# Optimization experiments

Hardware: AMD Instinct MI355X
Metric: run time of the kernel (lower is better)

The kernel has to match this reference:

```python
import jax, jax.numpy as jnp
import numpy as np

N, E, IN, H, C, OUT = 50000, 800000, 128, 4, 32, 40
HID = H * C  # 128


def _layernorm(x, g, b, eps=1e-5):
    mu = x.mean(-1, keepdims=True)
    var = ((x - mu) ** 2).mean(-1, keepdims=True)
    return (x - mu) * jax.lax.rsqrt(var + eps) * g + b


def _gatv2(x, src, dst, Wl, bl, Wr, br, att, bias, heads, ch, concat):
    n = x.shape[0]
    xl = (x @ Wl + bl).reshape(n, heads, ch)  # source-side transform
    xr = (x @ Wr + br).reshape(n, heads, ch)  # target-side transform
    e = jax.nn.leaky_relu(xl[src] + xr[dst], 0.2)          # [E,H,C]
    alpha = jnp.einsum('ehc,hc->eh', e, att)                # [E,H]
    m = jax.ops.segment_max(alpha, dst, num_segments=n)
    m = jnp.where(jnp.isfinite(m), m, 0.0)
    a = jnp.exp(alpha - m[dst])
    denom = jax.ops.segment_sum(a, dst, num_segments=n)
    a = a / (denom[dst] + 1e-16)
    out = jax.ops.segment_sum(xl[src] * a[:, :, None], dst, num_segments=n)  # [N,H,C]
    out = out.reshape(n, heads * ch) if concat else out.mean(1)
    return out + bias


def setup_inputs():
    key = jax.random.key(0)
    ks = jax.random.split(key, 26)
    s = 0.05
    rn = lambda k, sh: jax.random.normal(k, sh, jnp.float32) * s
    inp = {
        'x': jax.random.normal(ks[0], (N, IN), jnp.float32),
        'edge_index': jax.random.randint(ks[1], (2, E), 0, N, jnp.int64),
        'W0': rn(ks[2], (IN, HID)), 'b0': jnp.zeros((HID,), jnp.float32),
        'W1l': rn(ks[3], (IN, HID)), 'b1l': jnp.zeros((HID,), jnp.float32),
        'W1r': rn(ks[4], (IN, HID)), 'b1r': jnp.zeros((HID,), jnp.float32),
        'att1': rn(ks[5], (H, C)), 'bias1': jnp.zeros((HID,), jnp.float32),
        'g1': jnp.ones((HID,), jnp.float32), 'be1': jnp.zeros((HID,), jnp.float32),
        'W2l': rn(ks[6], (HID, HID)), 'b2l': jnp.zeros((HID,), jnp.float32),
        'W2r': rn(ks[7], (HID, HID)), 'b2r': jnp.zeros((HID,), jnp.float32),
        'att2': rn(ks[8], (H, C)), 'bias2': jnp.zeros((HID,), jnp.float32),
        'g2': jnp.ones((HID,), jnp.float32), 'be2': jnp.zeros((HID,), jnp.float32),
        'W3l': rn(ks[9], (HID, OUT)), 'b3l': jnp.zeros((OUT,), jnp.float32),
        'W3r': rn(ks[10], (HID, OUT)), 'b3r': jnp.zeros((OUT,), jnp.float32),
        'att3': rn(ks[11], (1, OUT)), 'bias3': jnp.zeros((OUT,), jnp.float32),
    }
    return inp


def reference(x, edge_index, W0, b0, W1l, b1l, W1r, b1r, att1, bias1, g1, be1,
              W2l, b2l, W2r, b2r, att2, bias2, g2, be2,
              W3l, b3l, W3r, b3r, att3, bias3):
    src, dst = edge_index[0], edge_index[1]
    identity = x @ W0 + b0
    out = _gatv2(x, src, dst, W1l, b1l, W1r, b1r, att1, bias1, H, C, True)
    out = jax.nn.gelu(_layernorm(out, g1, be1), approximate=False)
    x1 = out + identity  # dropout is identity in eval mode
    out = _gatv2(x1, src, dst, W2l, b2l, W2r, b2r, att2, bias2, H, C, True)
    out = jax.nn.gelu(_layernorm(out, g2, be2), approximate=False)
    x2 = out + x1
    return _gatv2(x2, src, dst, W3l, b3l, W3r, b3r, att3, bias3, 1, OUT, False)
```

## Files before the change

### kernel.cpp

```cpp
#include <hip/hip_runtime.h>
#include <hip/hip_bf16.h>

#define NN 50000
#define EE 800000
#define OUTD 40
#define NBUCK 196
#define BCAP 8192
#define ABLKS 400
#define EPB 2000

typedef __attribute__((ext_vector_type(8))) short short8;
typedef __attribute__((ext_vector_type(4))) float floatx4;

__device__ __forceinline__ float bf2f(unsigned short u) {
  union { unsigned int i; float f; } v; v.i = ((unsigned int)u) << 16; return v.f;
}
__device__ __forceinline__ unsigned short f2bf(float f) {
  union { float f; unsigned int i; } v; v.f = f;
  unsigned int x = v.i;
  return (unsigned short)((x + 0x7fffu + ((x >> 16) & 1u)) >> 16);
}
__device__ __forceinline__ float blo(unsigned int u) {
  union { unsigned int i; float f; } v; v.i = u << 16; return v.f;
}
__device__ __forceinline__ float bhi(unsigned int u) {
  union { unsigned int i; float f; } v; v.i = u & 0xffff0000u; return v.f;
}

template <int CTRL>
__device__ __forceinline__ float dpp_add(float x) {
  int y = __builtin_amdgcn_update_dpp(0, __float_as_int(x), CTRL, 0xF, 0xF, true);
  return x + __int_as_float(y);
}

__device__ __forceinline__ float gelu1(float y) {
  float y2 = y * y;
  float z = y * fmaf(0.0356774081f, y2, 0.7978845608f);
  float e = __expf(-2.f * z);
  float r = __builtin_amdgcn_rcpf(1.f + e);
  float th = fmaf(2.f, r, -1.f);
  return y * fmaf(0.5f, th, 0.5f);
}

__device__ __forceinline__ int clampe(int i, int last) {
  int r = i <= last ? i : last;
  return r < 0 ? 0 : r;
}

__device__ __forceinline__ int probe_f32(const void* x) {
  int lane = threadIdx.x & 63;
  unsigned short u = ((const unsigned short*)x)[2 * lane];
  int exf = (u >> 7) & 0xFF;
  unsigned long long b = __ballot((exf >= 100 && exf <= 142) ? 1 : 0);
  return (__popcll(b) >= 48) ? 0 : 1;
}
__device__ __forceinline__ int probe_i64(const void* ei) {
  int lane = threadIdx.x & 63;
  long long v = ((const long long*)ei)[lane];
  unsigned long long b = __ballot((v >= 0 && v < NN) ? 1 : 0);
  return (__popcll(b) >= 48) ? 1 : 0;
}

struct WDesc { const void* W; unsigned short* F; int T; int ncols; };
struct WDescs { WDesc d[7]; int cum[8]; };
struct PCv { const void* s; unsigned short* d; int n; int cap; };
struct PCvs { PCv a[17]; };

__global__ __launch_bounds__(256) void init_kernel(const void* __restrict__ ei,
                                                   const void* __restrict__ x,
                                                   int* __restrict__ flags,
                                                   int* __restrict__ bcur,
                                                   WDescs ds, PCvs P) {
  int b = blockIdx.x;
  int f32 = probe_f32(x);
  if (b < 48) {
    int idx = b * 256 + threadIdx.x;
    if (idx >= 12288) return;
    int mi = 0;
    while (idx >= ds.cum[mi + 1]) mi++;
    int local = idx - ds.cum[mi];
    WDesc d = ds.d[mi];
    int lane = local & 63;
    int rest = local >> 6;
    int t = rest % d.T;
    int kb = rest / d.T;
    int m = lane & 15, quad = lane >> 4;
    int col = t * 16 + m;
    short8 v;
    for (int j = 0; j < 8; ++j) {
      int k = kb * 32 + quad * 8 + j;
      if (col < d.ncols) {
        int off = k * d.ncols + col;
        v[j] = f32 ? (short)f2bf(((const float*)d.W)[off])
                   : (short)((const unsigned short*)d.W)[off];
      } else {
        v[j] = 0;
      }
    }
    *(short8*)(d.F + (size_t)local * 8) = v;
  } else if (b < 65) {
    PCv p = P.a[b - 48];
    for (int i = threadIdx.x; i < p.cap; i += 256) {
      unsigned short o = 0;
      if (i < p.n)
        o = f32 ? f2bf(((const float*)p.s)[i]) : ((const unsigned short*)p.s)[i];
      p.d[i] = o;
    }
  } else {
    for (int i = threadIdx.x; i < NBUCK * 16; i += 256) bcur[i] = 0;
    if (threadIdx.x < 64) {
      int i64 = probe_i64(ei);
      if (threadIdx.x == 0) {
        flags[0] = i64;
        flags[1] = f32;
        flags[2] = 0;
      }
    }
  }
}

struct GSet { const unsigned short* F; const unsigned short* bias; unsigned short* Out; };
struct GArgs { GSet s[3]; };

__device__ __forceinline__ short8 pack_f4(float4 u0, float4 u1) {
  short8 r;
  r[0] = (short)f2bf(u0.x); r[1] = (short)f2bf(u0.y);
  r[2] = (short)f2bf(u0.z); r[3] = (short)f2bf(u0.w);
  r[4] = (short)f2bf(u1.x); r[5] = (short)f2bf(u1.y);
  r[6] = (short)f2bf(u1.z); r[7] = (short)f2bf(u1.w);
  return r;
}

__device__ __forceinline__ void gemm_body(int wave, int lane, const void* __restrict__ A,
                                          int f32, const GArgs& g, int nset, int M,
                                          int T, int ncols) {
  int r0 = wave * 16;
  if (r0 >= M) return;
  int m = lane & 15, quad = lane >> 4;
  short8 a0, a1, a2, a3;
  if (!f32) {
    const unsigned short* ar = (const unsigned short*)A + (size_t)(r0 + m) * 128 + quad * 8;
    a0 = *(const short8*)(ar);
    a1 = *(const short8*)(ar + 32);
    a2 = *(const short8*)(ar + 64);
    a3 = *(const short8*)(ar + 96);
  } else {
    const float* ar = (const float*)A + (size_t)(r0 + m) * 128 + quad * 8;
    a0 = pack_f4(*(const float4*)(ar), *(const float4*)(ar + 4));
    a1 = pack_f4(*(const float4*)(ar + 32), *(const float4*)(ar + 36));
    a2 = pack_f4(*(const float4*)(ar + 64), *(const float4*)(ar + 68));
    a3 = pack_f4(*(const float4*)(ar + 96), *(const float4*)(ar + 100));
  }
  size_t kstride = (size_t)T * 64 * 8;
  for (int si = 0; si < nset; ++si) {
    const unsigned short* F = g.s[si].F;
    const unsigned short* bias = g.s[si].bias;
    unsigned short* Out = g.s[si].Out;
    for (int t = 0; t < T; ++t) {
      floatx4 acc = {0.f, 0.f, 0.f, 0.f};
      const unsigned short* wp = F + ((size_t)t * 64 + lane) * 8;
      acc = __builtin_amdgcn_mfma_f32_16x16x32_bf16(a0, *(const short8*)(wp), acc, 0, 0, 0);
      acc = __builtin_amdgcn_mfma_f32_16x16x32_bf16(a1, *(const short8*)(wp + kstride), acc, 0, 0, 0);
      acc = __builtin_amdgcn_mfma_f32_16x16x32_bf16(a2, *(const short8*)(wp + 2 * kstride), acc, 0, 0, 0);
      acc = __builtin_amdgcn_mfma_f32_16x16x32_bf16(a3, *(const short8*)(wp + 3 * kstride), acc, 0, 0, 0);
      int col = t * 16 + m;
      if (col < ncols) {
        float bb = bf2f(bias[col]);
        for (int r = 0; r < 4; ++r) {
          int row = r0 + quad * 4 + r;
          Out[(size_t)row * ncols + col] = f2bf(acc[r] + bb);
        }
      }
    }
  }
}

__global__ __launch_bounds__(256) void gemm_multi_kernel(
    const void* __restrict__ A, const int* __restrict__ flagp, GArgs g,
    int nset, int M, int T, int ncols) {
  int wave = blockIdx.x * 4 + (threadIdx.x >> 6);
  int lane = threadIdx.x & 63;
  gemm_body(wave, lane, A, *flagp, g, nset, M, T, ncols);
}

__global__ __launch_bounds__(512) void fused_scatter_gemm(
    const void* __restrict__ ei, unsigned int* __restrict__ bedges,
    int* __restrict__ bcur, const void* __restrict__ A,
    const int* __restrict__ flagp, GArgs g, int nset, int M, int T, int ncols) {
  __shared__ int lhist[NBUCK];
  __shared__ int lbase[NBUCK];
  if (blockIdx.x >= ABLKS) {
    int wave = (blockIdx.x - ABLKS) * 8 + (threadIdx.x >> 6);
    gemm_body(wave, threadIdx.x & 63, A, *flagp, g, nset, M, T, ncols);
    return;
  }
  int tid = threadIdx.x;
  if (tid < NBUCK) lhist[tid] = 0;
  int i64 = probe_i64(ei);
  __syncthreads();
  int e0 = blockIdx.x * EPB;
  int e1 = e0 + EPB; if (e1 > EE) e1 = EE;
  for (int e = e0 + tid; e < e1; e += 512) {
    int d = i64 ? (int)((const long long*)ei)[EE + e] : ((const int*)ei)[EE + e];
    d = d < 0 ? 0 : (d >= NN ? NN - 1 : d);
    atomicAdd(&lhist[d >> 8], 1);
  }
  __syncthreads();
  if (tid < NBUCK) {
    int c = lhist[tid];
    lbase[tid] = c ? atomicAdd(&bcur[tid * 16], c) : 0;
    lhist[tid] = 0;
  }
  __syncthreads();
  for (int e = e0 + tid; e < e1; e += 512) {
    int s, d;
    if (i64) {
      s = (int)((const long long*)ei)[e];
      d = (int)((const long long*)ei)[EE + e];
    } else {
      s = ((const int*)ei)[e];
      d = ((const int*)ei)[EE + e];
    }
    s = s < 0 ? 0 : (s >= NN ? NN - 1 : s);
    d = d < 0 ? 0 : (d >= NN ? NN - 1 : d);
    int bin = d >> 8;
    int r = atomicAdd(&lhist[bin], 1);
    int pos = lbase[bin] + r;
    if (pos < BCAP)
      bedges[(size_t)bin * BCAP + pos] =
          ((unsigned int)(d & 0xFF) << 24) | ((unsigned int)s << 8);
  }
}

__global__ __launch_bounds__(512) void fused_sort_gemm(
    const unsigned int* __restrict__ bedges, const int* __restrict__ bcur,
    int* __restrict__ offs, int* __restrict__ src_sorted,
    const void* __restrict__ A, const int* __restrict__ flagp, GArgs g,
    int nset, int M, int T, int ncols) {
  __shared__ int lhist[256];
  __shared__ int lscan[256];
  __shared__ int lbin[256];
  __shared__ int sbase, scount, stotal;
  __shared__ unsigned int le[BCAP];
  __shared__ unsigned short lrank[BCAP];
  if (blockIdx.x >= NBUCK) {
    int wave = (blockIdx.x - NBUCK) * 8 + (threadIdx.x >> 6);
    gemm_body(wave, threadIdx.x & 63, A, *flagp, g, nset, M, T, ncols);
    return;
  }
  int k = blockIdx.x;
  int tid = threadIdx.x;
  if (tid < 256) {
    int c = 0;
    if (tid < NBUCK) {
      int v = bcur[tid * 16];
      c = v < BCAP ? v : BCAP;
    }
    lscan[tid] = c;
  }
  __syncthreads();
  for (int off = 1; off < 256; off <<= 1) {
    int u = 0;
    if (tid < 256 && tid >= off) u = lscan[tid - off];
    __syncthreads();
    if (tid < 256) lscan[tid] += u;
    __syncthreads();
  }
  if (tid == 0) {
    int pb = (k == 0) ? 0 : lscan[k - 1];
    sbase = pb;
    scount = lscan[k] - pb;
    stotal = lscan[NBUCK - 1];
  }
  if (tid < 256) lhist[tid] = 0;
  __syncthreads();
  int base = sbase, count = scount;
  const unsigned int* myb = bedges + (size_t)k * BCAP;
  for (int i = tid; i < count; i += 512) {
    unsigned int pk = myb[i];
    int bin = pk >> 24;
    int r = atomicAdd(&lhist[bin], 1);
    le[i] = pk;
    lrank[i] = (unsigned short)r;
  }
  __syncthreads();
  int hc = 0;
  if (tid < 256) {
    hc = lhist[tid];
    lscan[tid] = hc;
  }
  __syncthreads();
  for (int off = 1; off < 256; off <<= 1) {
    int u = 0;
    if (tid < 256 && tid >= off) u = lscan[tid - off];
    __syncthreads();
    if (tid < 256) lscan[tid] += u;
    __syncthreads();
  }
  if (tid < 256) {
    int binoff = lscan[tid] - hc;
    lbin[tid] = binoff;
    int node = k * 256 + tid;
    if (node < NN) offs[node] = base + binoff;
    if (k == 0 && tid == 0) offs[NN] = stotal;
  }
  __syncthreads();
  for (int i = tid; i < count; i += 512) {
    unsigned int pk = le[i];
    int bin = pk >> 24;
    int pos = base + lbin[bin] + (int)lrank[i];
    src_sorted[pos] = (int)(pk & 0x00FFFF00u);
  }
}

__global__ __launch_bounds__(256) void edge_hid_kernel(
    const unsigned short* __restrict__ xl, const unsigned short* __restrict__ xr,
    const unsigned short* __restrict__ att, const unsigned short* __restrict__ bias,
    const unsigned short* __restrict__ gamma, const unsigned short* __restrict__ beta,
    const unsigned short* __restrict__ resid, unsigned short* __restrict__ xout,
    const int* __restrict__ offs, const int* __restrict__ srcs) {
  int wpair = blockIdx.x * 4 + (threadIdx.x >> 6);
  int lane = threadIdx.x & 63;
  int half = lane >> 5;
  int wv = wpair * 2 + half;
  if (wv >= NN) return;
  int hl = lane & 31;
  int sub = hl >> 4;
  int cb = (hl & 15) * 16;
  int beg = offs[wv], end = offs[wv + 1], last = end - 1;
  int iters = (end - beg + 1) >> 1;
  int oi = __shfl_xor(iters, 32);
  int maxit = __builtin_amdgcn_readfirstlane(iters > oi ? iters : oi);
  const char* xlb = (const char*)xl;
  int c0 = hl * 4;
  uint2 rr = *(const uint2*)(resid + (size_t)wv * 128 + c0);
  uint4 xr8 = *(const uint4*)((const char*)xr + (size_t)wv * 256 + cb);
  float rx0 = blo(xr8.x), rx1 = bhi(xr8.x), rx2 = blo(xr8.y), rx3 = bhi(xr8.y);
  float rx4 = blo(xr8.z), rx5 = bhi(xr8.z), rx6 = blo(xr8.w), rx7 = bhi(xr8.w);
  uint4 at8 = *(const uint4*)((const char*)att + cb);
  float a0 = blo(at8.x), a1 = bhi(at8.x), a2 = blo(at8.y), a3 = bhi(at8.y);
  float a4 = blo(at8.z), a5 = bhi(at8.z), a6 = blo(at8.w), a7 = bhi(at8.w);
  float acc0 = 0.f, acc1 = 0.f, acc2 = 0.f, acc3 = 0.f;
  float acc4 = 0.f, acc5 = 0.f, acc6 = 0.f, acc7 = 0.f, den = 0.f;
  int ir = beg + sub;
  int o_cur = srcs[clampe(ir, last)];
  int o_nxt = srcs[clampe(ir + 2, last)];
  uint4 u = *(const uint4*)(xlb + (o_cur + cb));
  for (int it = 0; it < maxit; ++it) {
    int o_p = srcs[clampe(ir + 4, last)];
    uint4 un = *(const uint4*)(xlb + (o_nxt + cb));
    float mk = (ir <= last) ? 1.f : 0.f;
    ir += 2;
    float x0 = blo(u.x), x1 = bhi(u.x), x2 = blo(u.y), x3 = bhi(u.y);
    float x4 = blo(u.z), x5 = bhi(u.z), x6 = blo(u.w), x7 = bhi(u.w);
    float t0 = x0 + rx0, t1 = x1 + rx1, t2 = x2 + rx2, t3 = x3 + rx3;
    float t4 = x4 + rx4, t5 = x5 + rx5, t6 = x6 + rx6, t7 = x7 + rx7;
    float pa = a0 * t0;
    pa = fmaf(a1, t1, pa); pa = fmaf(a2, t2, pa); pa = fmaf(a3, t3, pa);
    pa = fmaf(a4, t4, pa); pa = fmaf(a5, t5, pa); pa = fmaf(a6, t6, pa); pa = fmaf(a7, t7, pa);
    float pb = a0 * fabsf(t0);
    pb = fmaf(a1, fabsf(t1), pb); pb = fmaf(a2, fabsf(t2), pb); pb = fmaf(a3, fabsf(t3), pb);
    pb = fmaf(a4, fabsf(t4), pb); pb = fmaf(a5, fabsf(t5), pb);
    pb = fmaf(a6, fabsf(t6), pb); pb = fmaf(a7, fabsf(t7), pb);
    float p = fmaf(0.4f, pb, 0.6f * pa);
    p = dpp_add<0xB1>(p);
    p = dpp_add<0x4E>(p);
    float w = __expf(fminf(p, 60.f)) * mk;
    den += w;
    acc0 = fmaf(w, x0, acc0); acc1 = fmaf(w, x1, acc1);
    acc2 = fmaf(w, x2, acc2); acc3 = fmaf(w, x3, acc3);
    acc4 = fmaf(w, x4, acc4); acc5 = fmaf(w, x5, acc5);
    acc6 = fmaf(w, x6, acc6); acc7 = fmaf(w, x7, acc7);
    u = un;
    o_nxt = o_p;
  }
  den += __shfl_xor(den, 16);
  acc0 += __shfl_xor(acc0, 16); acc1 += __shfl_xor(acc1, 16);
  acc2 += __shfl_xor(acc2, 16); acc3 += __shfl_xor(acc3, 16);
  acc4 += __shfl_xor(acc4, 16); acc5 += __shfl_xor(acc5, 16);
  acc6 += __shfl_xor(acc6, 16); acc7 += __shfl_xor(acc7, 16);
  int srcLane = (half << 5) + (hl >> 1);
  float b0 = __shfl(acc0, srcLane), b1 = __shfl(acc1, srcLane);
  float b2 = __shfl(acc2, srcLane), b3 = __shfl(acc3, srcLane);
  float h4 = __shfl(acc4, srcLane), h5 = __shfl(acc5, srcLane);
  float h6 = __shfl(acc6, srcLane), h7 = __shfl(acc7, srcLane);
  float dn = __shfl(den, srcLane);
  bool hi = (hl & 1) != 0;
  float v0 = hi ? h4 : b0, v1 = hi ? h5 : b1, v2 = hi ? h6 : b2, v3 = hi ? h7 : b3;
  float inv = __builtin_amdgcn_rcpf(dn + 1e-16f);
  uint2 bb = *(const uint2*)(bias + c0);
  float o0 = v0 * inv + blo(bb.x), o1 = v1 * inv + bhi(bb.x);
  float o2 = v2 * inv + blo(bb.y), o3 = v3 * inv + bhi(bb.y);
  float s = (o0 + o1) + (o2 + o3);
  for (int k = 1; k < 32; k <<= 1) s += __shfl_xor(s, k);
  float mu = s * (1.f / 128.f);
  float d0 = o0 - mu, d1 = o1 - mu, d2 = o2 - mu, d3 = o3 - mu;
  float q = (d0 * d0 + d1 * d1) + (d2 * d2 + d3 * d3);
  for (int k = 1; k < 32; k <<= 1) q += __shfl_xor(q, k);
  float rstd = rsqrtf(q * (1.f / 128.f) + 1e-5f);
  uint2 gg = *(const uint2*)(gamma + c0);
  uint2 be = *(const uint2*)(beta + c0);
  float y0 = d0 * rstd * blo(gg.x) + blo(be.x);
  float y1 = d1 * rstd * bhi(gg.x) + bhi(be.x);
  float y2 = d2 * rstd * blo(gg.y) + blo(be.y);
  float y3 = d3 * rstd * bhi(gg.y) + bhi(be.y);
  y0 = gelu1(y0); y1 = gelu1(y1); y2 = gelu1(y2); y3 = gelu1(y3);
  y0 += blo(rr.x); y1 += bhi(rr.x); y2 += blo(rr.y); y3 += bhi(rr.y);
  uint2 pk;
  pk.x = (unsigned int)f2bf(y0) | ((unsigned int)f2bf(y1) << 16);
  pk.y = (unsigned int)f2bf(y2) | ((unsigned int)f2bf(y3) << 16);
  *(uint2*)(xout + (size_t)wv * 128 + c0) = pk;
}

__global__ __launch_bounds__(256) void edge_out_kernel(
    const unsigned short* __restrict__ xl, const unsigned short* __restrict__ xr,
    const unsigned short* __restrict__ att, const unsigned short* __restrict__ bias,
    void* __restrict__ out, const int* __restrict__ flagp,
    const int* __restrict__ offs, const int* __restrict__ srcs) {
  int wv = blockIdx.x * 4 + (threadIdx.x >> 6);
  if (wv >= NN) return;
  int lane = threadIdx.x & 63;
  int oct = lane >> 3;
  int cb = (lane & 7) * 16;
  int beg = __builtin_amdgcn_readfirstlane(offs[wv]);
  int last = __builtin_amdgcn_readfirstlane(offs[wv + 1]) - 1;
  const char* xlb = (const char*)xl;
  uint4 xr8 = *(const uint4*)((const char*)xr + (size_t)wv * 128 + cb);
  float rx0 = blo(xr8.x), rx1 = bhi(xr8.x), rx2 = blo(xr8.y), rx3 = bhi(xr8.y);
  float rx4 = blo(xr8.z), rx5 = bhi(xr8.z), rx6 = blo(xr8.w), rx7 = bhi(xr8.w);
  uint4 at8 = *(const uint4*)((const char*)att + cb);
  float a0 = blo(at8.x), a1 = bhi(at8.x), a2 = blo(at8.y), a3 = bhi(at8.y);
  float a4 = blo(at8.z), a5 = bhi(at8.z), a6 = blo(at8.w), a7 = bhi(at8.w);
  float acc0 = 0.f, acc1 = 0.f, acc2 = 0.f, acc3 = 0.f;
  float acc4 = 0.f, acc5 = 0.f, acc6 = 0.f, acc7 = 0.f, den = 0.f;
  int ir = beg + oct;
  int o_cur = srcs[clampe(ir, last)];
  int o_nxt = srcs[clampe(ir + 8, last)];
  uint4 u = *(const uint4*)(xlb + ((o_cur >> 1) + cb));
  for (int e = beg; e <= last; e += 8) {
    int o_p = srcs[clampe(ir + 16, last)];
    uint4 un = *(const uint4*)(xlb + ((o_nxt >> 1) + cb));
    float mk = (ir <= last) ? 1.f : 0.f;
    ir += 8;
    float x0 = blo(u.x), x1 = bhi(u.x), x2 = blo(u.y), x3 = bhi(u.y);
    float x4 = blo(u.z), x5 = bhi(u.z), x6 = blo(u.w), x7 = bhi(u.w);
    float t0 = x0 + rx0, t1 = x1 + rx1, t2 = x2 + rx2, t3 = x3 + rx3;
    float t4 = x4 + rx4, t5 = x5 + rx5, t6 = x6 + rx6, t7 = x7 + rx7;
    float pa = a0 * t0;
    pa = fmaf(a1, t1, pa); pa = fmaf(a2, t2, pa); pa = fmaf(a3, t3, pa);
    pa = fmaf(a4, t4, pa); pa = fmaf(a5, t5, pa); pa = fmaf(a6, t6, pa); pa = fmaf(a7, t7, pa);
    float pb = a0 * fabsf(t0);
    pb = fmaf(a1, fabsf(t1), pb); pb = fmaf(a2, fabsf(t2), pb); pb = fmaf(a3, fabsf(t3), pb);
    pb = fmaf(a4, fabsf(t4), pb); pb = fmaf(a5, fabsf(t5), pb);
    pb = fmaf(a6, fabsf(t6), pb); pb = fmaf(a7, fabsf(t7), pb);
    float p = fmaf(0.4f, pb, 0.6f * pa);
    p = dpp_add<0xB1>(p);
    p = dpp_add<0x4E>(p);
    p = dpp_add<0x141>(p);
    float w = __expf(fminf(p, 60.f)) * mk;
    den += w;
    acc0 = fmaf(w, x0, acc0); acc1 = fmaf(w, x1, acc1);
    acc2 = fmaf(w, x2, acc2); acc3 = fmaf(w, x3, acc3);
    acc4 = fmaf(w, x4, acc4); acc5 = fmaf(w, x5, acc5);
    acc6 = fmaf(w, x6, acc6); acc7 = fmaf(w, x7, acc7);
    u = un;
    o_nxt = o_p;
  }
  den += __shfl_xor(den, 8);  den += __shfl_xor(den, 16);  den += __shfl_xor(den, 32);
  acc0 += __shfl_xor(acc0, 8); acc0 += __shfl_xor(acc0, 16); acc0 += __shfl_xor(acc0, 32);
  acc1 += __shfl_xor(acc1, 8); acc1 += __shfl_xor(acc1, 16); acc1 += __shfl_xor(acc1, 32);
  acc2 += __shfl_xor(acc2, 8); acc2 += __shfl_xor(acc2, 16); acc2 += __shfl_xor(acc2, 32);
  acc3 += __shfl_xor(acc3, 8); acc3 += __shfl_xor(acc3, 16); acc3 += __shfl_xor(acc3, 32);
  acc4 += __shfl_xor(acc4, 8); acc4 += __shfl_xor(acc4, 16); acc4 += __shfl_xor(acc4, 32);
  acc5 += __shfl_xor(acc5, 8); acc5 += __shfl_xor(acc5, 16); acc5 += __shfl_xor(acc5, 32);
  acc6 += __shfl_xor(acc6, 8); acc6 += __shfl_xor(acc6, 16); acc6 += __shfl_xor(acc6, 32);
  acc7 += __shfl_xor(acc7, 8); acc7 += __shfl_xor(acc7, 16); acc7 += __shfl_xor(acc7, 32);
  float inv = __builtin_amdgcn_rcpf(den + 1e-16f);
  if (lane < 5) {
    uint4 bb = *(const uint4*)((const char*)bias + cb);
    float v0 = acc0 * inv + blo(bb.x), v1 = acc1 * inv + bhi(bb.x);
    float v2 = acc2 * inv + blo(bb.y), v3 = acc3 * inv + bhi(bb.y);
    float v4 = acc4 * inv + blo(bb.z), v5 = acc5 * inv + bhi(bb.z);
    float v6 = acc6 * inv + blo(bb.w), v7 = acc7 * inv + bhi(bb.w);
    int c0 = lane * 8;
    if (*flagp) {
      float* op = (float*)out + (size_t)wv * OUTD + c0;
      float4 f0 = {v0, v1, v2, v3};
      float4 f1 = {v4, v5, v6, v7};
      *(float4*)(op) = f0;
      *(float4*)(op + 4) = f1;
    } else {
      uint4 pk;
      pk.x = (unsigned int)f2bf(v0) | ((unsigned int)f2bf(v1) << 16);
      pk.y = (unsigned int)f2bf(v2) | ((unsigned int)f2bf(v3) << 16);
      pk.z = (unsigned int)f2bf(v4) | ((unsigned int)f2bf(v5) << 16);
      pk.w = (unsigned int)f2bf(v6) | ((unsigned int)f2bf(v7) << 16);
      *(uint4*)((unsigned short*)out + (size_t)wv * OUTD + c0) = pk;
    }
  }
}

extern "C" void kernel_launch(void* const* d_in, const int* in_sizes, int n_in,
                              void* d_out, int out_size, void* d_ws, size_t ws_size,
                              hipStream_t stream) {
  const void* x = d_in[0];
  const void* ei = d_in[1];

  char* ws = (char*)d_ws;
  size_t o = 0;
  auto alloc = [&](size_t bytes) {
    void* p = ws + o;
    o = (o + bytes + 255) & ~(size_t)255;
    return p;
  };
  int* flags = (int*)alloc(256);
  int* src_sorted = (int*)alloc((size_t)EE * 4);
  int* offs = (int*)alloc((size_t)(NN + 1) * 4);
  int* bcur = (int*)alloc((size_t)NBUCK * 16 * 4);
  unsigned int* bedges = (unsigned int*)alloc((size_t)NBUCK * BCAP * 4);
  unsigned short* F_W0 = (unsigned short*)alloc(2048 * 16);
  unsigned short* F_W1l = (unsigned short*)alloc(2048 * 16);
  unsigned short* F_W1r = (unsigned short*)alloc(2048 * 16);
  unsigned short* F_W2l = (unsigned short*)alloc(2048 * 16);
  unsigned short* F_W2r = (unsigned short*)alloc(2048 * 16);
  unsigned short* F_W3l = (unsigned short*)alloc(1024 * 16);
  unsigned short* F_W3r = (unsigned short*)alloc(1024 * 16);
  unsigned short* pblk = (unsigned short*)alloc(4096);
  unsigned short* ident = (unsigned short*)alloc((size_t)NN * 128 * 2);
  unsigned short* bxl = (unsigned short*)alloc((size_t)NN * 128 * 2);
  unsigned short* bxr = (unsigned short*)alloc((size_t)NN * 128 * 2);
  (void)ws_size;

  unsigned short* pb0 = pblk;
  unsigned short* pb1l = pblk + 128;
  unsigned short* pb1r = pblk + 256;
  unsigned short* patt1 = pblk + 384;
  unsigned short* pbias1 = pblk + 512;
  unsigned short* pg1 = pblk + 640;
  unsigned short* pbe1 = pblk + 768;
  unsigned short* pb2l = pblk + 896;
  unsigned short* pb2r = pblk + 1024;
  unsigned short* patt2 = pblk + 1152;
  unsigned short* pbias2 = pblk + 1280;
  unsigned short* pg2 = pblk + 1408;
  unsigned short* pbe2 = pblk + 1536;
  unsigned short* pb3l = pblk + 1664;
  unsigned short* pb3r = pblk + 1728;
  unsigned short* patt3 = pblk + 1792;
  unsigned short* pbias3 = pblk + 1856;

  WDescs wd;
  wd.d[0] = {d_in[2], F_W0, 8, 128};
  wd.d[1] = {d_in[4], F_W1l, 8, 128};
  wd.d[2] = {d_in[6], F_W1r, 8, 128};
  wd.d[3] = {d_in[12], F_W2l, 8, 128};
  wd.d[4] = {d_in[14], F_W2r, 8, 128};
  wd.d[5] = {d_in[20], F_W3l, 4, 40};
  wd.d[6] = {d_in[22], F_W3r, 4, 40};
  int cum[8] = {0, 2048, 4096, 6144, 8192, 10240, 11264, 12288};
  for (int i = 0; i < 8; ++i) wd.cum[i] = cum[i];
  PCvs P;
  P.a[0] = {d_in[3], pb0, 128, 128};
  P.a[1] = {d_in[5], pb1l, 128, 128};
  P.a[2] = {d_in[7], pb1r, 128, 128};
  P.a[3] = {d_in[8], patt1, 128, 128};
  P.a[4] = {d_in[9], pbias1, 128, 128};
  P.a[5] = {d_in[10], pg1, 128, 128};
  P.a[6] = {d_in[11], pbe1, 128, 128};
  P.a[7] = {d_in[13], pb2l, 128, 128};
  P.a[8] = {d_in[15], pb2r, 128, 128};
  P.a[9] = {d_in[16], patt2, 128, 128};
  P.a[10] = {d_in[17], pbias2, 128, 128};
  P.a[11] = {d_in[18], pg2, 128, 128};
  P.a[12] = {d_in[19], pbe2, 128, 128};
  P.a[13] = {d_in[21], pb3l, 40, 64};
  P.a[14] = {d_in[23], pb3r, 40, 64};
  P.a[15] = {d_in[24], patt3, 40, 64};
  P.a[16] = {d_in[25], pbias3, 40, 64};
  init_kernel<<<66, 256, 0, stream>>>(ei, x, flags, bcur, wd, P);

  const int* fx = flags + 1;
  const int* f0 = flags + 2;
  const int gb8 = (NN + 127) / 128;
  const int gb4 = (NN / 16 + 3) / 4;
  const int eb = (NN + 3) / 4;
  const int eb2 = (NN / 2 + 3) / 4;

  GArgs gi; gi.s[0] = {F_W0, pb0, ident};
  gi.s[1] = {nullptr, nullptr, nullptr}; gi.s[2] = {nullptr, nullptr, nullptr};
  fused_scatter_gemm<<<ABLKS + gb8, 512, 0, stream>>>(ei, bedges, bcur, x, fx, gi, 1,
                                                      NN, 8, 128);

  GArgs g1a; g1a.s[0] = {F_W1l, pb1l, bxl}; g1a.s[1] = {F_W1r, pb1r, bxr};
  g1a.s[2] = {nullptr, nullptr, nullptr};
  fused_sort_gemm<<<NBUCK + gb8, 512, 0, stream>>>(bedges, bcur, offs, src_sorted, x,
                                                   fx, g1a, 2, NN, 8, 128);

  edge_hid_kernel<<<eb2, 256, 0, stream>>>(bxl, bxr, patt1, pbias1, pg1, pbe1, ident,
                                           ident, offs, src_sorted);

  GArgs g2a; g2a.s[0] = {F_W2l, pb2l, bxl}; g2a.s[1] = {F_W2r, pb2r, bxr};
  g2a.s[2] = {nullptr, nullptr, nullptr};
  gemm_multi_kernel<<<gb4, 256, 0, stream>>>(ident, f0, g2a, 2, NN, 8, 128);
  edge_hid_kernel<<<eb2, 256, 0, stream>>>(bxl, bxr, patt2, pbias2, pg2, pbe2, ident,
                                           ident, offs, src_sorted);

  GArgs g3a; g3a.s[0] = {F_W3l, pb3l, bxl}; g3a.s[1] = {F_W3r, pb3r, bxr};
  g3a.s[2] = {nullptr, nullptr, nullptr};
  gemm_multi_kernel<<<gb4, 256, 0, stream>>>(ident, f0, g3a, 2, NN, 4, 64);
  edge_out_kernel<<<eb, 256, 0, stream>>>(bxl, bxr, patt3, pbias3, d_out, fx, offs,
                                          src_sorted);
}
```

Before: 306.4 us.

## Cache bf16 copy of x and vectorize GEMM output stores via swapped MFMA operands

The first GEMM, which reads the fp32 input x, now also writes a bf16 copy of x to a new workspace buffer. The second fused GEMM reads that copy, so it moves half the bytes and skips re-packing. The MFMA operands are swapped so each lane holds four consecutive output columns of one row. The epilogue can then load the bias as one uint2 and write four packed bf16 values per lane in a single 8-byte store, replacing four strided 2-byte stores. The cost is an extra 12.8MB write in the first kernel and a dependency on kernel ordering for the cache.

Result: slower. 322.3 us (+5.2%).

```diff
diff --git a/kernel.cpp b/kernel.cpp
--- a/kernel.cpp
+++ b/kernel.cpp
@@ -133,7 +133,8 @@
 
 __device__ __forceinline__ void gemm_body(int wave, int lane, const void* __restrict__ A,
                                           int f32, const GArgs& g, int nset, int M,
-                                          int T, int ncols) {
+                                          int T, int ncols,
+                                          unsigned short* __restrict__ Acache) {
   int r0 = wave * 16;
   if (r0 >= M) return;
   int m = lane & 15, quad = lane >> 4;
@@ -150,6 +151,13 @@
     a1 = pack_f4(*(const float4*)(ar + 32), *(const float4*)(ar + 36));
     a2 = pack_f4(*(const float4*)(ar + 64), *(const float4*)(ar + 68));
     a3 = pack_f4(*(const float4*)(ar + 96), *(const float4*)(ar + 100));
+    if (Acache) {
+      unsigned short* cp = Acache + (size_t)(r0 + m) * 128 + quad * 8;
+      *(short8*)(cp) = a0;
+      *(short8*)(cp + 32) = a1;
+      *(short8*)(cp + 64) = a2;
+      *(short8*)(cp + 96) = a3;
+    }
   }
   size_t kstride = (size_t)T * 64 * 8;
   for (int si = 0; si < nset; ++si) {
@@ -159,17 +167,19 @@
     for (int t = 0; t < T; ++t) {
       floatx4 acc = {0.f, 0.f, 0.f, 0.f};
       const unsigned short* wp = F + ((size_t)t * 64 + lane) * 8;
-      acc = __builtin_amdgcn_mfma_f32_16x16x32_bf16(a0, *(const short8*)(wp), acc, 0, 0, 0);
-      acc = __builtin_amdgcn_mfma_f32_16x16x32_bf16(a1, *(const short8*)(wp + kstride), acc, 0, 0, 0);
-      acc = __builtin_amdgcn_mfma_f32_16x16x32_bf16(a2, *(const short8*)(wp + 2 * kstride), acc, 0, 0, 0);
-      acc = __builtin_amdgcn_mfma_f32_16x16x32_bf16(a3, *(const short8*)(wp + 3 * kstride), acc, 0, 0, 0);
-      int col = t * 16 + m;
-      if (col < ncols) {
-        float bb = bf2f(bias[col]);
-        for (int r = 0; r < 4; ++r) {
-          int row = r0 + quad * 4 + r;
-          Out[(size_t)row * ncols + col] = f2bf(acc[r] + bb);
-        }
+      acc = __builtin_amdgcn_mfma_f32_16x16x32_bf16(*(const short8*)(wp), a0, acc, 0, 0, 0);
+      acc = __builtin_amdgcn_mfma_f32_16x16x32_bf16(*(const short8*)(wp + kstride), a1, acc, 0, 0, 0);
+      acc = __builtin_amdgcn_mfma_f32_16x16x32_bf16(*(const short8*)(wp + 2 * kstride), a2, acc, 0, 0, 0);
+      acc = __builtin_amdgcn_mfma_f32_16x16x32_bf16(*(const short8*)(wp + 3 * kstride), a3, acc, 0, 0, 0);
+      int cbase = t * 16 + quad * 4;
+      if (cbase < ncols) {
+        uint2 bb = *(const uint2*)(bias + cbase);
+        float v0 = acc[0] + blo(bb.x), v1 = acc[1] + bhi(bb.x);
+        float v2 = acc[2] + blo(bb.y), v3 = acc[3] + bhi(bb.y);
+        uint2 pk;
+        pk.x = (unsigned int)f2bf(v0) | ((unsigned int)f2bf(v1) << 16);
+        pk.y = (unsigned int)f2bf(v2) | ((unsigned int)f2bf(v3) << 16);
+        *(uint2*)(Out + (size_t)(r0 + m) * ncols + cbase) = pk;
       }
     }
   }
@@ -180,18 +190,21 @@
     int nset, int M, int T, int ncols) {
   int wave = blockIdx.x * 4 + (threadIdx.x >> 6);
   int lane = threadIdx.x & 63;
-  gemm_body(wave, lane, A, *flagp, g, nset, M, T, ncols);
+  gemm_body(wave, lane, A, *flagp, g, nset, M, T, ncols, nullptr);
 }
 
 __global__ __launch_bounds__(512) void fused_scatter_gemm(
     const void* __restrict__ ei, unsigned int* __restrict__ bedges,
     int* __restrict__ bcur, const void* __restrict__ A,
-    const int* __restrict__ flagp, GArgs g, int nset, int M, int T, int ncols) {
+    const int* __restrict__ flagp, GArgs g, int nset, int M, int T, int ncols,
+    unsigned short* __restrict__ Acache) {
   __shared__ int lhist[NBUCK];
   __shared__ int lbase[NBUCK];
   if (blockIdx.x >= ABLKS) {
     int wave = (blockIdx.x - ABLKS) * 8 + (threadIdx.x >> 6);
-    gemm_body(wave, threadIdx.x & 63, A, *flagp, g, nset, M, T, ncols);
+    int f32 = *flagp;
+    gemm_body(wave, threadIdx.x & 63, A, f32, g, nset, M, T, ncols,
+              f32 ? Acache : nullptr);
     return;
   }
   int tid = threadIdx.x;
@@ -236,7 +249,7 @@
     const unsigned int* __restrict__ bedges, const int* __restrict__ bcur,
     int* __restrict__ offs, int* __restrict__ src_sorted,
     const void* __restrict__ A, const int* __restrict__ flagp, GArgs g,
-    int nset, int M, int T, int ncols) {
+    int nset, int M, int T, int ncols, const unsigned short* __restrict__ Acache) {
   __shared__ int lhist[256];
   __shared__ int lscan[256];
   __shared__ int lbin[256];
@@ -245,7 +258,9 @@
   __shared__ unsigned short lrank[BCAP];
   if (blockIdx.x >= NBUCK) {
     int wave = (blockIdx.x - NBUCK) * 8 + (threadIdx.x >> 6);
-    gemm_body(wave, threadIdx.x & 63, A, *flagp, g, nset, M, T, ncols);
+    int f32 = *flagp;
+    const void* Ause = f32 ? (const void*)Acache : A;
+    gemm_body(wave, threadIdx.x & 63, Ause, 0, g, nset, M, T, ncols, nullptr);
     return;
   }
   int k = blockIdx.x;
@@ -529,6 +544,7 @@
   unsigned short* ident = (unsigned short*)alloc((size_t)NN * 128 * 2);
   unsigned short* bxl = (unsigned short*)alloc((size_t)NN * 128 * 2);
   unsigned short* bxr = (unsigned short*)alloc((size_t)NN * 128 * 2);
+  unsigned short* xbf = (unsigned short*)alloc((size_t)NN * 128 * 2);
   (void)ws_size;
 
   unsigned short* pb0 = pblk;
@@ -589,12 +605,12 @@
   GArgs gi; gi.s[0] = {F_W0, pb0, ident};
   gi.s[1] = {nullptr, nullptr, nullptr}; gi.s[2] = {nullptr, nullptr, nullptr};
   fused_scatter_gemm<<<ABLKS + gb8, 512, 0, stream>>>(ei, bedges, bcur, x, fx, gi, 1,
-                                                      NN, 8, 128);
+                                                      NN, 8, 128, xbf);
 
   GArgs g1a; g1a.s[0] = {F_W1l, pb1l, bxl}; g1a.s[1] = {F_W1r, pb1r, bxr};
   g1a.s[2] = {nullptr, nullptr, nullptr};
   fused_sort_gemm<<<NBUCK + gb8, 512, 0, stream>>>(bedges, bcur, offs, src_sorted, x,
-                                                   fx, g1a, 2, NN, 8, 128);
+                                                   fx, g1a, 2, NN, 8, 128, xbf);
 
   edge_hid_kernel<<<eb2, 256, 0, stream>>>(bxl, bxr, patt1, pbias1, pg1, pbe1, ident,
                                            ident, offs, src_sorted);
```

## Fuse next-layer GEMMs into edge_hid epilogue with ping-pong buffers

Applied to the files above, without the earlier changes.

Each edge_hid block now stages its 8 normalized output rows in shared memory, zero-padded to 16 rows. It then runs MFMA against the next layer's left and right weight fragments, writing the next xl/xr directly. This removes the two standalone gemm_multi launches and the global round-trip of the activation matrix, and skips writing x2 since nothing downstream reads it. In exchange, every block re-reads the full weight fragments from cache and wastes half of each 16-row MFMA tile. Ping-pong xl/xr buffers avoid overwriting inputs still being gathered by other blocks.

Result: no change. 306.6 us (+0.1%).

```diff
diff --git a/kernel.cpp b/kernel.cpp
--- a/kernel.cpp
+++ b/kernel.cpp
@@ -175,14 +175,6 @@
   }
 }
 
-__global__ __launch_bounds__(256) void gemm_multi_kernel(
-    const void* __restrict__ A, const int* __restrict__ flagp, GArgs g,
-    int nset, int M, int T, int ncols) {
-  int wave = blockIdx.x * 4 + (threadIdx.x >> 6);
-  int lane = threadIdx.x & 63;
-  gemm_body(wave, lane, A, *flagp, g, nset, M, T, ncols);
-}
-
 __global__ __launch_bounds__(512) void fused_scatter_gemm(
     const void* __restrict__ ei, unsigned int* __restrict__ bedges,
     int* __restrict__ bcur, const void* __restrict__ A,
@@ -313,17 +305,21 @@
   }
 }
 
+template <int TT, int NCOLS, int WRITEX>
 __global__ __launch_bounds__(256) void edge_hid_kernel(
     const unsigned short* __restrict__ xl, const unsigned short* __restrict__ xr,
     const unsigned short* __restrict__ att, const unsigned short* __restrict__ bias,
     const unsigned short* __restrict__ gamma, const unsigned short* __restrict__ beta,
     const unsigned short* __restrict__ resid, unsigned short* __restrict__ xout,
-    const int* __restrict__ offs, const int* __restrict__ srcs) {
+    const int* __restrict__ offs, const int* __restrict__ srcs,
+    const unsigned short* __restrict__ Fl, const unsigned short* __restrict__ Fr,
+    const unsigned short* __restrict__ bl, const unsigned short* __restrict__ br,
+    unsigned short* __restrict__ outl, unsigned short* __restrict__ outr) {
+  __shared__ unsigned short sA[16 * 128];
   int wpair = blockIdx.x * 4 + (threadIdx.x >> 6);
   int lane = threadIdx.x & 63;
   int half = lane >> 5;
   int wv = wpair * 2 + half;
-  if (wv >= NN) return;
   int hl = lane & 31;
   int sub = hl >> 4;
   int cb = (hl & 15) * 16;
@@ -409,7 +405,44 @@
   uint2 pk;
   pk.x = (unsigned int)f2bf(y0) | ((unsigned int)f2bf(y1) << 16);
   pk.y = (unsigned int)f2bf(y2) | ((unsigned int)f2bf(y3) << 16);
-  *(uint2*)(xout + (size_t)wv * 128 + c0) = pk;
+  if (WRITEX) *(uint2*)(xout + (size_t)wv * 128 + c0) = pk;
+
+  int lrow = (threadIdx.x >> 6) * 2 + half;
+  *(uint2*)(&sA[lrow * 128 + c0]) = pk;
+  *(uint2*)(&sA[1024 + threadIdx.x * 4]) = make_uint2(0, 0);
+  __syncthreads();
+  int m = lane & 15, quad = lane >> 4;
+  const unsigned short* arow = sA + m * 128 + quad * 8;
+  short8 A0 = *(const short8*)(arow);
+  short8 A1 = *(const short8*)(arow + 32);
+  short8 A2 = *(const short8*)(arow + 64);
+  short8 A3 = *(const short8*)(arow + 96);
+  const size_t kst = (size_t)TT * 64 * 8;
+  const int rowbase = blockIdx.x * 8;
+  const int wid = threadIdx.x >> 6;
+  constexpr int PER = (2 * TT) / 4;
+#pragma unroll
+  for (int jj = 0; jj < PER; ++jj) {
+    int j = wid * PER + jj;
+    bool isr = j >= TT;
+    const unsigned short* F = isr ? Fr : Fl;
+    const unsigned short* bs = isr ? br : bl;
+    unsigned short* Out = isr ? outr : outl;
+    int t = isr ? j - TT : j;
+    floatx4 acc = {0.f, 0.f, 0.f, 0.f};
+    const unsigned short* wp = F + ((size_t)t * 64 + lane) * 8;
+    acc = __builtin_amdgcn_mfma_f32_16x16x32_bf16(A0, *(const short8*)(wp), acc, 0, 0, 0);
+    acc = __builtin_amdgcn_mfma_f32_16x16x32_bf16(A1, *(const short8*)(wp + kst), acc, 0, 0, 0);
+    acc = __builtin_amdgcn_mfma_f32_16x16x32_bf16(A2, *(const short8*)(wp + 2 * kst), acc, 0, 0, 0);
+    acc = __builtin_amdgcn_mfma_f32_16x16x32_bf16(A3, *(const short8*)(wp + 3 * kst), acc, 0, 0, 0);
+    int col = t * 16 + m;
+    float bbv = bf2f(bs[col]);
+    if (quad < 2) {
+#pragma unroll
+      for (int r = 0; r < 4; ++r)
+        Out[(size_t)(rowbase + quad * 4 + r) * NCOLS + col] = f2bf(acc[r] + bbv);
+    }
+  }
 }
 
 __global__ __launch_bounds__(256) void edge_out_kernel(
@@ -527,8 +560,10 @@
   unsigned short* F_W3r = (unsigned short*)alloc(1024 * 16);
   unsigned short* pblk = (unsigned short*)alloc(4096);
   unsigned short* ident = (unsigned short*)alloc((size_t)NN * 128 * 2);
-  unsigned short* bxl = (unsigned short*)alloc((size_t)NN * 128 * 2);
-  unsigned short* bxr = (unsigned short*)alloc((size_t)NN * 128 * 2);
+  unsigned short* bxlA = (unsigned short*)alloc((size_t)NN * 128 * 2);
+  unsigned short* bxrA = (unsigned short*)alloc((size_t)NN * 128 * 2);
+  unsigned short* bxlB = (unsigned short*)alloc((size_t)NN * 128 * 2);
+  unsigned short* bxrB = (unsigned short*)alloc((size_t)NN * 128 * 2);
   (void)ws_size;
 
   unsigned short* pb0 = pblk;
@@ -580,9 +615,7 @@
   init_kernel<<<66, 256, 0, stream>>>(ei, x, flags, bcur, wd, P);
 
   const int* fx = flags + 1;
-  const int* f0 = flags + 2;
   const int gb8 = (NN + 127) / 128;
-  const int gb4 = (NN / 16 + 3) / 4;
   const int eb = (NN + 3) / 4;
   const int eb2 = (NN / 2 + 3) / 4;
 
@@ -591,23 +624,19 @@
   fused_scatter_gemm<<<ABLKS + gb8, 512, 0, stream>>>(ei, bedges, bcur, x, fx, gi, 1,
                                                       NN, 8, 128);
 
-  GArgs g1a; g1a.s[0] = {F_W1l, pb1l, bxl}; g1a.s[1] = {F_W1r, pb1r, bxr};
+  GArgs g1a; g1a.s[0] = {F_W1l, pb1l, bxlA}; g1a.s[1] = {F_W1r, pb1r, bxrA};
   g1a.s[2] = {nullptr, nullptr, nullptr};
   fused_sort_gemm<<<NBUCK + gb8, 512, 0, stream>>>(bedges, bcur, offs, src_sorted, x,
                                                    fx, g1a, 2, NN, 8, 128);
 
-  edge_hid_kernel<<<eb2, 256, 0, stream>>>(bxl, bxr, patt1, pbias1, pg1, pbe1, ident,
-                                           ident, offs, src_sorted);
-
-  GArgs g2a; g2a.s[0] = {F_W2l, pb2l, bxl}; g2a.s[1] = {F_W2r, pb2r, bxr};
-  g2a.s[2] = {nullptr, nullptr, nullptr};
-  gemm_multi_kernel<<<gb4, 256, 0, stream>>>(ident, f0, g2a, 2, NN, 8, 128);
-  edge_hid_kernel<<<eb2, 256, 0, stream>>>(bxl, bxr, patt2, pbias2, pg2, pbe2, ident,
-                                           ident, offs, src_sorted);
-
-  GArgs g3a; g3a.s[0] = {F_W3l, pb3l, bxl}; g3a.s[1] = {F_W3r, pb3r, bxr};
-  g3a.s[2] = {nullptr, nullptr, nullptr};
-  gemm_multi_kernel<<<gb4, 256, 0, stream>>>(ident, f0, g3a, 2, NN, 4, 64);
-  edge_out_kernel<<<eb, 256, 0, stream>>>(bxl, bxr, patt3, pbias3, d_out, fx, offs,
+  edge_hid_kernel<8, 128, 1><<<eb2, 256, 0, stream>>>(
+      bxlA, bxrA, patt1, pbias1, pg1, pbe1, ident, ident, offs, src_sorted,
+      F_W2l, F_W2r, pb2l, pb2r, bxlB, bxrB);
+
+  edge_hid_kernel<4, 64, 0><<<eb2, 256, 0, stream>>>(
+      bxlB, bxrB, patt2, pbias2, pg2, pbe2, ident, ident, offs, src_sorted,
+      F_W3l, F_W3r, pb3l, pb3r, bxlA, bxrA);
+
+  edge_out_kernel<<<eb, 256, 0, stream>>>(bxlA, bxrA, patt3, pbias3, d_out, fx, offs,
                                           src_sorted);
 }
```
